# Kernel optimization log

Hardware: AMD Instinct MI355X
Metric: run time of the kernel (lower is better)

The kernel has to match this reference:

```python
import jax, jax.numpy as jnp
import numpy as np

NUM_USERS = 100000
USER_EMB_DIM = 64
PROC_DIM = 128          # Dense(128) embedding_processor
NUM_SHARDS = 16
MEM_SIZE = 512          # memory slots per shard
WORD_SIZE = 64
NUM_READS = 4
INPUT_SIZE = 256
B, S = 256, 128
IN_DIM = INPUT_SIZE + PROC_DIM  # combined controller input width


def setup_inputs() -> dict:
    key = jax.random.key(0)
    k = jax.random.split(key, 7)
    x = jax.random.normal(k[0], (B, S, INPUT_SIZE), dtype=jnp.float32)
    user_id = jax.random.randint(k[1], (B,), 0, NUM_USERS, dtype=jnp.int64)
    user_emb_table = jax.random.normal(k[2], (NUM_USERS, USER_EMB_DIM), dtype=jnp.float32) * 0.02
    W_proc = jax.random.normal(k[3], (USER_EMB_DIM, PROC_DIM), dtype=jnp.float32) * (1.0 / np.sqrt(USER_EMB_DIM))
    b_proc = jnp.zeros((PROC_DIM,), dtype=jnp.float32)
    # per-shard parameters: query projection + memory matrix (the shard's state)
    Wq = jax.random.normal(k[4], (NUM_SHARDS, IN_DIM, NUM_READS * WORD_SIZE), dtype=jnp.float32) * (1.0 / np.sqrt(IN_DIM))
    memory = jax.random.normal(k[5], (NUM_SHARDS, MEM_SIZE, WORD_SIZE), dtype=jnp.float32)
    return {"x": x, "user_id": user_id, "user_emb_table": user_emb_table,
            "W_proc": W_proc, "b_proc": b_proc, "Wq": Wq, "memory": memory}


def reference(x, user_id, user_emb_table, W_proc, b_proc, Wq, memory):
    # user embedding lookup + Dense processor
    ue = user_emb_table[user_id]                       # [B, E]
    pe = ue @ W_proc + b_proc                          # [B, PROC_DIM]
    # broadcast the processed embedding across the sequence and concat on features
    pe_seq = jnp.broadcast_to(pe[:, None, :], (x.shape[0], x.shape[1], pe.shape[-1]))
    combined = jnp.concatenate([x, pe_seq], axis=-1)   # [B, S, IN_DIM]
    # shard routing (irregular gather of per-shard params)
    sid = user_id % NUM_SHARDS                         # [B]
    Wq_g = Wq[sid]                                     # [B, IN_DIM, R*W]
    mem_g = memory[sid]                                # [B, M, W]
    # per-sample shard forward: content-based read
    q = jnp.einsum('bsi,bio->bso', combined, Wq_g)     # [B, S, R*W]
    q = q.reshape(q.shape[0], q.shape[1], NUM_READS, WORD_SIZE)
    scores = jnp.einsum('bsrw,bmw->bsrm', q, mem_g)    # [B, S, R, M]
    wts = jax.nn.softmax(scores, axis=-1)
    read_words = jnp.einsum('bsrm,bmw->bsrw', wts, mem_g)  # [B, S, R, W]
    # original code keeps final_states[-1] (last sample's state)
    final_state = wts[-1]                              # [S, R, M]
    return read_words, final_state
```

## Files before the change

kernel.cpp:

```cpp
#include <hip/hip_runtime.h>
#include <math.h>

#define BB 256
#define SSEQ 128
#define INPUT 256
#define PD 128
#define EE 64
#define RW 256
#define MM 512
#define WW 64
#define KD 384

typedef _Float16 half8 __attribute__((ext_vector_type(8)));
typedef __fp16 fp16x2 __attribute__((ext_vector_type(2)));
typedef float float4v __attribute__((ext_vector_type(4)));

#define LOG2E 1.44269504088896f
#define OUT1 8388608u

#define MEMT_OFF 65536
#define F32_OFF  131072
#define LDS_BYTES (131072 + 6144)
#define UE_O 0
#define PE_O 64
#define QPE_O 192
#define QP_O 448

union H8 { half8 h8; unsigned int u[4]; uint4 u4; };

__device__ __forceinline__ unsigned int pk2(float a, float b) {
    union { fp16x2 h; unsigned int u; } p;
    p.h = __builtin_amdgcn_cvt_pkrtz(a, b);
    return p.u;
}

__global__ void __launch_bounds__(1024, 4)
attn_kernel(const float* __restrict__ x, const int* __restrict__ user_id,
            const float* __restrict__ uet, const float* __restrict__ W_proc,
            const float* __restrict__ b_proc, const float* __restrict__ Wq,
            const float* __restrict__ memG, float* __restrict__ out)
{
    extern __shared__ char smraw[];
    unsigned short* smemu = (unsigned short*)smraw;
    unsigned int*   smw   = (unsigned int*)smraw;
    uint4*          sm128 = (uint4*)smraw;
    float*          smf   = (float*)(smraw + F32_OFF);

    const int t = threadIdx.x;
    const int b = blockIdx.x;
    const int lane = t & 63, wv = t >> 6;
    const int n16 = lane & 15, quad = lane >> 4;
    const int r = wv & 3, sq = wv >> 2;
    const int s0 = sq * 32;
    const int swz = n16 & 7;

    const int uid = user_id[b];
    const int sid = uid & 15;
    const float* memB = memG + (size_t)sid * (MM*WW);
    const float* wqX  = Wq + (size_t)sid * KD * RW;

    if (t < EE) smf[UE_O + t] = uet[(size_t)uid*EE + t];

    for (int i = 0; i < 32; ++i) {
        int idx = i*1024 + t;
        int n = idx & 255, kp = idx >> 8;
        float w0 = wqX[(size_t)(2*kp)    *RW + n];
        float w1 = wqX[(size_t)(2*kp + 1)*RW + n];
        smw[((((kp>>2)*256 + n) << 2) | (kp & 3))] = pk2(w0, w1);
    }
    __syncthreads();

    if (t < PD) {
        float a = b_proc[t];
        #pragma unroll
        for (int e = 0; e < EE; ++e) a = fmaf(smf[UE_O + e], W_proc[e*PD + t], a);
        smf[PE_O + t] = a;
    }
    __syncthreads();
    {
        int n = t & 255, h = t >> 8;
        float s = 0.f;
        const float* wr = wqX + (size_t)(256 + h*32)*RW + n;
        #pragma unroll 8
        for (int k = 0; k < 32; ++k) s = fmaf(smf[PE_O + h*32 + k], wr[(size_t)k*RW], s);
        smf[QP_O + h*256 + n] = s;
    }
    __syncthreads();
    if (t < 256) smf[QPE_O + t] = LOG2E * (smf[QP_O + t] + smf[QP_O + 256 + t]
                                         + smf[QP_O + 512 + t] + smf[QP_O + 768 + t]);
    __syncthreads();

    float4v qacc[4][2];
    #pragma unroll
    for (int mt = 0; mt < 4; ++mt)
        #pragma unroll
        for (int nt = 0; nt < 2; ++nt) qacc[mt][nt] = (float4v)0.f;

    const float* xB = x + (size_t)(b*SSEQ + s0) * INPUT;
    for (int kc = 0; kc < 8; ++kc) {
        H8 afr[4];
        #pragma unroll
        for (int mt = 0; mt < 4; ++mt)
            afr[mt].u4 = sm128[(kc*4 + quad)*256 + r*64 + mt*16 + n16];
        H8 bfr[2];
        #pragma unroll
        for (int nt = 0; nt < 2; ++nt) {
            const float* xg = xB + (size_t)(nt*16 + n16)*INPUT + kc*32 + quad*8;
            float4 a0 = *(const float4*)xg;
            float4 a1 = *(const float4*)(xg + 4);
            bfr[nt].u[0] = pk2(a0.x*LOG2E, a0.y*LOG2E);
            bfr[nt].u[1] = pk2(a0.z*LOG2E, a0.w*LOG2E);
            bfr[nt].u[2] = pk2(a1.x*LOG2E, a1.y*LOG2E);
            bfr[nt].u[3] = pk2(a1.z*LOG2E, a1.w*LOG2E);
        }
        #pragma unroll
        for (int mt = 0; mt < 4; ++mt)
            #pragma unroll
            for (int nt = 0; nt < 2; ++nt)
                qacc[mt][nt] = __builtin_amdgcn_mfma_f32_16x16x32_f16(afr[mt].h8, bfr[nt].h8, qacc[mt][nt], 0, 0, 0);
    }
    #pragma unroll
    for (int mt = 0; mt < 4; ++mt)
        #pragma unroll
        for (int reg = 0; reg < 4; ++reg) {
            float qv = smf[QPE_O + r*64 + mt*16 + quad*4 + reg];
            #pragma unroll
            for (int nt = 0; nt < 2; ++nt) qacc[mt][nt][reg] += qv;
        }
    unsigned int pkq[4][2][2];
    #pragma unroll
    for (int mt = 0; mt < 4; ++mt)
        #pragma unroll
        for (int nt = 0; nt < 2; ++nt) {
            pkq[mt][nt][0] = pk2(qacc[mt][nt][0], qacc[mt][nt][1]);
            pkq[mt][nt][1] = pk2(qacc[mt][nt][2], qacc[mt][nt][3]);
        }
    unsigned int bq[2][2][4];
    #pragma unroll
    for (int kc2 = 0; kc2 < 2; ++kc2)
        #pragma unroll
        for (int nt = 0; nt < 2; ++nt)
            #pragma unroll
            for (int p = 0; p < 4; ++p) {
                int qp = ((quad & 1) << 1) | (p >> 1);
                int src = n16 + (qp << 4);
                int sr = p & 1;
                int lo  = __shfl((int)pkq[kc2*2    ][nt][sr], src, 64);
                int hiv = __shfl((int)pkq[kc2*2 + 1][nt][sr], src, 64);
                bq[kc2][nt][p] = (unsigned int)((quad < 2) ? lo : hiv);
            }
    __syncthreads();

    for (int i = 0; i < 4; ++i) {
        int id = t + i*1024;
        int m = id >> 3, cw = id & 7;
        const float* g = memB + m*64 + cw*8;
        float4 a0 = *(const float4*)g;
        float4 a1 = *(const float4*)(g + 4);
        sm128[m*8 + (cw ^ (m & 7))] =
            make_uint4(pk2(a0.x,a0.y), pk2(a0.z,a0.w), pk2(a1.x,a1.y), pk2(a1.z,a1.w));
    }
    __syncthreads();
    for (int i = 0; i < 4; ++i) {
        int id = t + i*1024;
        int w = id & 63, cm = id >> 6;
        unsigned int uu[4];
        #pragma unroll
        for (int p = 0; p < 4; ++p) {
            int m0 = cm*8 + 2*p, m1 = m0 + 1;
            unsigned short lo = smemu[m0*64 + (((w>>3) ^ (m0&7))<<3) + (w&7)];
            unsigned short hi = smemu[m1*64 + (((w>>3) ^ (m1&7))<<3) + (w&7)];
            uu[p] = (unsigned int)lo | ((unsigned int)hi << 16);
        }
        sm128[(MEMT_OFF >> 4) + w*64 + (cm ^ (w & 7))] = make_uint4(uu[0],uu[1],uu[2],uu[3]);
    }
    __syncthreads();

    float4v Oa[4][2];
    #pragma unroll
    for (int wt = 0; wt < 4; ++wt)
        #pragma unroll
        for (int nt = 0; nt < 2; ++nt) Oa[wt][nt] = (float4v)0.f;
    float Ml[2] = {-1e30f, -1e30f}, ll[2] = {0.f, 0.f};

    for (int mtile = 0; mtile < 16; ++mtile) {
        float4v Sa[2][2];
        #pragma unroll
        for (int msub = 0; msub < 2; ++msub)
            #pragma unroll
            for (int nt = 0; nt < 2; ++nt) Sa[msub][nt] = (float4v)0.f;
        #pragma unroll
        for (int msub = 0; msub < 2; ++msub) {
            int m = mtile*32 + msub*16 + n16;
            #pragma unroll
            for (int kc2 = 0; kc2 < 2; ++kc2) {
                H8 af; af.u4 = sm128[m*8 + ((kc2*4 + quad) ^ swz)];
                #pragma unroll
                for (int nt = 0; nt < 2; ++nt) {
                    H8 bf; bf.u[0]=bq[kc2][nt][0]; bf.u[1]=bq[kc2][nt][1];
                           bf.u[2]=bq[kc2][nt][2]; bf.u[3]=bq[kc2][nt][3];
                    Sa[msub][nt] = __builtin_amdgcn_mfma_f32_16x16x32_f16(af.h8, bf.h8, Sa[msub][nt], 0, 0, 0);
                }
            }
        }
        unsigned int pkP[2][2][2];
        #pragma unroll
        for (int nt = 0; nt < 2; ++nt) {
            float tm = Sa[0][nt][0];
            #pragma unroll
            for (int g = 1; g < 4; ++g) tm = fmaxf(tm, Sa[0][nt][g]);
            #pragma unroll
            for (int g = 0; g < 4; ++g) tm = fmaxf(tm, Sa[1][nt][g]);
            tm = fmaxf(tm, __shfl_xor(tm, 16, 64));
            tm = fmaxf(tm, __shfl_xor(tm, 32, 64));
            float Mn = fmaxf(Ml[nt], tm);
            float al = __builtin_amdgcn_exp2f(Ml[nt] - Mn);
            float pv[2][4]; float ts = 0.f;
            #pragma unroll
            for (int msub = 0; msub < 2; ++msub)
                #pragma unroll
                for (int g = 0; g < 4; ++g) {
                    pv[msub][g] = __builtin_amdgcn_exp2f(Sa[msub][nt][g] - Mn);
                    ts += pv[msub][g];
                }
            ts += __shfl_xor(ts, 16, 64);
            ts += __shfl_xor(ts, 32, 64);
            ll[nt] = al*ll[nt] + ts;
            Ml[nt] = Mn;
            pkP[0][nt][0] = pk2(pv[0][0], pv[0][1]); pkP[0][nt][1] = pk2(pv[0][2], pv[0][3]);
            pkP[1][nt][0] = pk2(pv[1][0], pv[1][1]); pkP[1][nt][1] = pk2(pv[1][2], pv[1][3]);
            #pragma unroll
            for (int wt = 0; wt < 4; ++wt)
                #pragma unroll
                for (int g = 0; g < 4; ++g) Oa[wt][nt][g] *= al;
        }
        unsigned int bp[2][4];
        #pragma unroll
        for (int nt = 0; nt < 2; ++nt)
            #pragma unroll
            for (int p = 0; p < 4; ++p) {
                int qp = ((quad & 1) << 1) | (p >> 1);
                int src = n16 + (qp << 4);
                int sr = p & 1;
                int lo  = __shfl((int)pkP[0][nt][sr], src, 64);
                int hiv = __shfl((int)pkP[1][nt][sr], src, 64);
                bp[nt][p] = (unsigned int)((quad < 2) ? lo : hiv);
            }
        #pragma unroll
        for (int wt = 0; wt < 4; ++wt) {
            H8 af; af.u4 = sm128[(MEMT_OFF >> 4) + (wt*16 + n16)*64 + ((mtile*4 + quad) ^ swz)];
            #pragma unroll
            for (int nt = 0; nt < 2; ++nt) {
                H8 bf; bf.u[0]=bp[nt][0]; bf.u[1]=bp[nt][1]; bf.u[2]=bp[nt][2]; bf.u[3]=bp[nt][3];
                Oa[wt][nt] = __builtin_amdgcn_mfma_f32_16x16x32_f16(af.h8, bf.h8, Oa[wt][nt], 0, 0, 0);
            }
        }
    }

    #pragma unroll
    for (int nt = 0; nt < 2; ++nt) {
        float inv = 1.0f / ll[nt];
        int s = s0 + nt*16 + n16;
        #pragma unroll
        for (int wt = 0; wt < 4; ++wt) {
            float4 o = make_float4(Oa[wt][nt][0]*inv, Oa[wt][nt][1]*inv,
                                   Oa[wt][nt][2]*inv, Oa[wt][nt][3]*inv);
            *(float4*)&out[((size_t)(b*SSEQ + s)*4 + r)*WW + wt*16 + quad*4] = o;
        }
    }

    if (b == BB - 1) {
        for (int mtile = 0; mtile < 16; ++mtile) {
            float4v Sa[2][2];
            #pragma unroll
            for (int msub = 0; msub < 2; ++msub)
                #pragma unroll
                for (int nt = 0; nt < 2; ++nt) Sa[msub][nt] = (float4v)0.f;
            #pragma unroll
            for (int msub = 0; msub < 2; ++msub) {
                int m = mtile*32 + msub*16 + n16;
                #pragma unroll
                for (int kc2 = 0; kc2 < 2; ++kc2) {
                    H8 af; af.u4 = sm128[m*8 + ((kc2*4 + quad) ^ swz)];
                    #pragma unroll
                    for (int nt = 0; nt < 2; ++nt) {
                        H8 bf; bf.u[0]=bq[kc2][nt][0]; bf.u[1]=bq[kc2][nt][1];
                               bf.u[2]=bq[kc2][nt][2]; bf.u[3]=bq[kc2][nt][3];
                        Sa[msub][nt] = __builtin_amdgcn_mfma_f32_16x16x32_f16(af.h8, bf.h8, Sa[msub][nt], 0, 0, 0);
                    }
                }
            }
            #pragma unroll
            for (int nt = 0; nt < 2; ++nt) {
                float inv = 1.0f / ll[nt];
                int s = s0 + nt*16 + n16;
                size_t base = (size_t)OUT1 + ((size_t)(s*4 + r) << 9);
                #pragma unroll
                for (int msub = 0; msub < 2; ++msub) {
                    float4 w4 = make_float4(
                        __builtin_amdgcn_exp2f(Sa[msub][nt][0] - Ml[nt]) * inv,
                        __builtin_amdgcn_exp2f(Sa[msub][nt][1] - Ml[nt]) * inv,
                        __builtin_amdgcn_exp2f(Sa[msub][nt][2] - Ml[nt]) * inv,
                        __builtin_amdgcn_exp2f(Sa[msub][nt][3] - Ml[nt]) * inv);
                    *(float4*)&out[base + mtile*32 + msub*16 + quad*4] = w4;
                }
            }
        }
    }
}

extern "C" void kernel_launch(void* const* d_in, const int* in_sizes, int n_in,
                              void* d_out, int out_size, void* d_ws, size_t ws_size,
                              hipStream_t stream) {
    const float* x    = (const float*)d_in[0];
    const int*   uid  = (const int*)  d_in[1];
    const float* uet  = (const float*)d_in[2];
    const float* Wp   = (const float*)d_in[3];
    const float* bp   = (const float*)d_in[4];
    const float* Wq   = (const float*)d_in[5];
    const float* mem  = (const float*)d_in[6];
    float* out = (float*)d_out;

    (void)hipFuncSetAttribute((const void*)attn_kernel,
                              hipFuncAttributeMaxDynamicSharedMemorySize, LDS_BYTES);
    attn_kernel<<<BB, 1024, LDS_BYTES, stream>>>(x, uid, uet, Wp, bp, Wq, mem, out);
}
```

Baseline: 168.7 us.

## Replace online softmax with two-pass max-then-accumulate softmax

Splits the memory-read attention into a first pass that computes scores only to find each row's maximum, then a second pass that recomputes scores and accumulates exp-weighted reads with a fixed max. This removes per-tile accumulator rescaling, the alpha exponentials and per-tile cross-lane reductions, at the cost of recomputing the query-memory score MFMAs. The last block now writes raw scores to the output during the main loop and normalises them in place from global memory, instead of running a separate recompute loop.

```diff
diff --git a/kernel.cpp b/kernel.cpp
--- a/kernel.cpp
+++ b/kernel.cpp
@@ -53,6 +53,7 @@
     const int r = wv & 3, sq = wv >> 2;
     const int s0 = sq * 32;
     const int swz = n16 & 7;
+    const bool blast = (b == BB - 1);
 
     const int uid = user_id[b];
     const int sid = uid & 15;
@@ -176,13 +177,7 @@
     }
     __syncthreads();
 
-    float4v Oa[4][2];
-    #pragma unroll
-    for (int wt = 0; wt < 4; ++wt)
-        #pragma unroll
-        for (int nt = 0; nt < 2; ++nt) Oa[wt][nt] = (float4v)0.f;
-    float Ml[2] = {-1e30f, -1e30f}, ll[2] = {0.f, 0.f};
-
+    float mxl[2] = {-1e30f, -1e30f};
     for (int mtile = 0; mtile < 16; ++mtile) {
         float4v Sa[2][2];
         #pragma unroll
@@ -203,36 +198,71 @@
                 }
             }
         }
+        #pragma unroll
+        for (int nt = 0; nt < 2; ++nt)
+            #pragma unroll
+            for (int msub = 0; msub < 2; ++msub)
+                #pragma unroll
+                for (int g = 0; g < 4; ++g) mxl[nt] = fmaxf(mxl[nt], Sa[msub][nt][g]);
+    }
+    float M[2];
+    #pragma unroll
+    for (int nt = 0; nt < 2; ++nt) {
+        float m0 = fmaxf(mxl[nt], __shfl_xor(mxl[nt], 16, 64));
+        M[nt] = fmaxf(m0, __shfl_xor(m0, 32, 64));
+    }
+
+    float4v Oa[4][2];
+    #pragma unroll
+    for (int wt = 0; wt < 4; ++wt)
+        #pragma unroll
+        for (int nt = 0; nt < 2; ++nt) Oa[wt][nt] = (float4v)0.f;
+    float llp[2] = {0.f, 0.f};
+
+    for (int mtile = 0; mtile < 16; ++mtile) {
+        float4v Sa[2][2];
+        #pragma unroll
+        for (int msub = 0; msub < 2; ++msub)
+            #pragma unroll
+            for (int nt = 0; nt < 2; ++nt) Sa[msub][nt] = (float4v)0.f;
+        #pragma unroll
+        for (int msub = 0; msub < 2; ++msub) {
+            int m = mtile*32 + msub*16 + n16;
+            #pragma unroll
+            for (int kc2 = 0; kc2 < 2; ++kc2) {
+                H8 af; af.u4 = sm128[m*8 + ((kc2*4 + quad) ^ swz)];
+                #pragma unroll
+                for (int nt = 0; nt < 2; ++nt) {
+                    H8 bf; bf.u[0]=bq[kc2][nt][0]; bf.u[1]=bq[kc2][nt][1];
+                           bf.u[2]=bq[kc2][nt][2]; bf.u[3]=bq[kc2][nt][3];
+                    Sa[msub][nt] = __builtin_amdgcn_mfma_f32_16x16x32_f16(af.h8, bf.h8, Sa[msub][nt], 0, 0, 0);
+                }
+            }
+        }
+        if (blast) {
+            #pragma unroll
+            for (int nt = 0; nt < 2; ++nt) {
+                int s = s0 + nt*16 + n16;
+                size_t base = (size_t)OUT1 + ((size_t)(s*4 + r) << 9) + mtile*32 + quad*4;
+                #pragma unroll
+                for (int msub = 0; msub < 2; ++msub)
+                    *(float4*)&out[base + msub*16] =
+                        make_float4(Sa[msub][nt][0], Sa[msub][nt][1], Sa[msub][nt][2], Sa[msub][nt][3]);
+            }
+        }
         unsigned int pkP[2][2][2];
         #pragma unroll
         for (int nt = 0; nt < 2; ++nt) {
-            float tm = Sa[0][nt][0];
-            #pragma unroll
-            for (int g = 1; g < 4; ++g) tm = fmaxf(tm, Sa[0][nt][g]);
-            #pragma unroll
-            for (int g = 0; g < 4; ++g) tm = fmaxf(tm, Sa[1][nt][g]);
-            tm = fmaxf(tm, __shfl_xor(tm, 16, 64));
-            tm = fmaxf(tm, __shfl_xor(tm, 32, 64));
-            float Mn = fmaxf(Ml[nt], tm);
-            float al = __builtin_amdgcn_exp2f(Ml[nt] - Mn);
-            float pv[2][4]; float ts = 0.f;
+            float pv[2][4];
             #pragma unroll
             for (int msub = 0; msub < 2; ++msub)
                 #pragma unroll
                 for (int g = 0; g < 4; ++g) {
-                    pv[msub][g] = __builtin_amdgcn_exp2f(Sa[msub][nt][g] - Mn);
-                    ts += pv[msub][g];
+                    pv[msub][g] = __builtin_amdgcn_exp2f(Sa[msub][nt][g] - M[nt]);
+                    llp[nt] += pv[msub][g];
                 }
-            ts += __shfl_xor(ts, 16, 64);
-            ts += __shfl_xor(ts, 32, 64);
-            ll[nt] = al*ll[nt] + ts;
-            Ml[nt] = Mn;
             pkP[0][nt][0] = pk2(pv[0][0], pv[0][1]); pkP[0][nt][1] = pk2(pv[0][2], pv[0][3]);
             pkP[1][nt][0] = pk2(pv[1][0], pv[1][1]); pkP[1][nt][1] = pk2(pv[1][2], pv[1][3]);
-            #pragma unroll
-            for (int wt = 0; wt < 4; ++wt)
-                #pragma unroll
-                for (int g = 0; g < 4; ++g) Oa[wt][nt][g] *= al;
         }
         unsigned int bp[2][4];
         #pragma unroll
@@ -259,7 +289,10 @@
 
     #pragma unroll
     for (int nt = 0; nt < 2; ++nt) {
-        float inv = 1.0f / ll[nt];
+        float ll = llp[nt];
+        ll += __shfl_xor(ll, 16, 64);
+        ll += __shfl_xor(ll, 32, 64);
+        float inv = 1.0f / ll;
         int s = s0 + nt*16 + n16;
         #pragma unroll
         for (int wt = 0; wt < 4; ++wt) {
@@ -269,42 +302,33 @@
         }
     }
 
-    if (b == BB - 1) {
-        for (int mtile = 0; mtile < 16; ++mtile) {
-            float4v Sa[2][2];
-            #pragma unroll
-            for (int msub = 0; msub < 2; ++msub)
-                #pragma unroll
-                for (int nt = 0; nt < 2; ++nt) Sa[msub][nt] = (float4v)0.f;
-            #pragma unroll
-            for (int msub = 0; msub < 2; ++msub) {
-                int m = mtile*32 + msub*16 + n16;
-                #pragma unroll
-                for (int kc2 = 0; kc2 < 2; ++kc2) {
-                    H8 af; af.u4 = sm128[m*8 + ((kc2*4 + quad) ^ swz)];
-                    #pragma unroll
-                    for (int nt = 0; nt < 2; ++nt) {
-                        H8 bf; bf.u[0]=bq[kc2][nt][0]; bf.u[1]=bq[kc2][nt][1];
-                               bf.u[2]=bq[kc2][nt][2]; bf.u[3]=bq[kc2][nt][3];
-                        Sa[msub][nt] = __builtin_amdgcn_mfma_f32_16x16x32_f16(af.h8, bf.h8, Sa[msub][nt], 0, 0, 0);
-                    }
-                }
-            }
-            #pragma unroll
-            for (int nt = 0; nt < 2; ++nt) {
-                float inv = 1.0f / ll[nt];
-                int s = s0 + nt*16 + n16;
-                size_t base = (size_t)OUT1 + ((size_t)(s*4 + r) << 9);
-                #pragma unroll
-                for (int msub = 0; msub < 2; ++msub) {
-                    float4 w4 = make_float4(
-                        __builtin_amdgcn_exp2f(Sa[msub][nt][0] - Ml[nt]) * inv,
-                        __builtin_amdgcn_exp2f(Sa[msub][nt][1] - Ml[nt]) * inv,
-                        __builtin_amdgcn_exp2f(Sa[msub][nt][2] - Ml[nt]) * inv,
-                        __builtin_amdgcn_exp2f(Sa[msub][nt][3] - Ml[nt]) * inv);
-                    *(float4*)&out[base + mtile*32 + msub*16 + quad*4] = w4;
-                }
-            }
+    if (blast) {
+        __threadfence();
+        __syncthreads();
+        const int row = t >> 1, half = t & 1;
+        float* rp = out + OUT1 + ((size_t)row << 9) + (half << 8);
+        float mx = -1e30f;
+        for (int i = 0; i < 64; ++i) {
+            float4 v = *(float4*)&rp[i*4];
+            mx = fmaxf(mx, fmaxf(fmaxf(v.x, v.y), fmaxf(v.z, v.w)));
+        }
+        mx = fmaxf(mx, __shfl_xor(mx, 1, 64));
+        float sum = 0.f;
+        for (int i = 0; i < 64; ++i) {
+            float4 v = *(float4*)&rp[i*4];
+            v.x = __builtin_amdgcn_exp2f(v.x - mx);
+            v.y = __builtin_amdgcn_exp2f(v.y - mx);
+            v.z = __builtin_amdgcn_exp2f(v.z - mx);
+            v.w = __builtin_amdgcn_exp2f(v.w - mx);
+            sum += v.x + v.y + v.z + v.w;
+            *(float4*)&rp[i*4] = v;
+        }
+        sum += __shfl_xor(sum, 1, 64);
+        float inv2 = 1.0f / sum;
+        for (int i = 0; i < 64; ++i) {
+            float4 v = *(float4*)&rp[i*4];
+            v.x *= inv2; v.y *= inv2; v.z *= inv2; v.w *= inv2;
+            *(float4*)&rp[i*4] = v;
         }
     }
 }
```

Measured after the change: 439.6 us. +160.5%, slower.
